# Kernel tuning notes

Hardware: AMD Instinct MI355X
Metric: run time of the kernel (lower is better)

## Reference

```python
import jax, jax.numpy as jnp
import numpy as np

PROCESSING_STEPS = 3


def setup_inputs() -> dict:
    key = jax.random.key(0)
    ks = jax.random.split(key, 8)
    B, N, d = 1024, 128, 128
    y = jax.random.normal(ks[0], (B, N, d), dtype=jnp.float32)
    lengths = jax.random.randint(ks[1], (B,), 1, N + 1, dtype=jnp.int32)
    s = 0.05
    W_ih = jax.random.normal(ks[2], (4 * d, 2 * d), dtype=jnp.float32) * s
    W_hh = jax.random.normal(ks[3], (4 * d, d), dtype=jnp.float32) * s
    b_ih = jax.random.normal(ks[4], (4 * d,), dtype=jnp.float32) * s
    b_hh = jax.random.normal(ks[5], (4 * d,), dtype=jnp.float32) * s
    W_m = jax.random.normal(ks[6], (1, 2 * d), dtype=jnp.float32) * s
    b_m = jax.random.normal(ks[7], (1,), dtype=jnp.float32) * s
    mean = jnp.zeros((1,), jnp.float32)
    stddev = jnp.ones((1,), jnp.float32)
    return {"y": y, "lengths": lengths, "W_ih": W_ih, "W_hh": W_hh,
            "b_ih": b_ih, "b_hh": b_hh, "W_m": W_m, "b_m": b_m,
            "mean": mean, "stddev": stddev}


def reference(y, lengths, W_ih, W_hh, b_ih, b_hh, W_m, b_m, mean, stddev):
    # y: [B, N, d] padded atomwise representation; lengths: valid atoms per molecule
    B, N, d = y.shape
    mask = jnp.arange(N)[None, :] < lengths[:, None]          # [B, N]
    maskf = mask.astype(y.dtype)[..., None]                    # [B, N, 1]
    neg_inf = jnp.finfo(y.dtype).min

    q_star = jnp.zeros((B, 2 * d), y.dtype)
    h = jnp.zeros((B, d), y.dtype)
    c = jnp.zeros((B, d), y.dtype)

    def step(carry, _):
        q_star, h, c = carry
        # single-layer LSTM cell (PyTorch gate order i, f, g, o)
        gates = q_star @ W_ih.T + b_ih + h @ W_hh.T + b_hh     # [B, 4d]
        i, f, g, o = jnp.split(gates, 4, axis=-1)
        c2 = jax.nn.sigmoid(f) * c + jax.nn.sigmoid(i) * jnp.tanh(g)
        h2 = jax.nn.sigmoid(o) * jnp.tanh(c2)
        q = h2                                                  # [B, d]
        # attention: gather q per atom, segment softmax, scatter_add
        e = jnp.einsum('bnd,bd->bn', y, q)                      # [B, N]
        e = jnp.where(mask, e, neg_inf)
        a = jax.nn.softmax(e, axis=-1)[..., None] * maskf       # [B, N, 1]
        r = jnp.sum(a * y, axis=1)                              # [B, d]
        return (jnp.concatenate([q, r], axis=-1), h2, c2), None

    (q_star, h, c), _ = jax.lax.scan(step, (q_star, h, c), None,
                                     length=PROCESSING_STEPS)
    out = q_star @ W_m.T + b_m                                  # [B, 1]
    return out * stddev + mean
```

## Files before the change

### kernel.cpp

```cpp
#include <hip/hip_runtime.h>
#include <math.h>

#define BB 1024
#define NN 128
#define DD 128

__device__ __forceinline__ float sigmoidf_(float x) { return 1.0f / (1.0f + expf(-x)); }

__global__ __launch_bounds__(256) void k_prep2(
    const float* __restrict__ W_ih, const float* __restrict__ W_hh,
    const float* __restrict__ b_ih, const float* __restrict__ b_hh,
    float* __restrict__ Wfull, float* __restrict__ gbase) {
  int b = blockIdx.x, t = threadIdx.x;
  if (b < 64) {
    int base = b * 2048;
    for (int i = t; i < 2048; i += 256) {
      int idx = base + i;
      int j = idx >> 8, d = idx & 255;
      float v = W_ih[(j << 8) + d];
      if (d < 128) v += W_hh[(j << 7) + d];
      Wfull[idx] = v;
    }
  } else {
    __shared__ float h1l[DD];
    if (t < DD) {
      float bi = b_ih[t] + b_hh[t];
      float bg = b_ih[256 + t] + b_hh[256 + t];
      float bo = b_ih[384 + t] + b_hh[384 + t];
      float cc = sigmoidf_(bi) * tanhf(bg);
      h1l[t] = sigmoidf_(bo) * tanhf(cc);
    }
    __syncthreads();
    int j0 = (b - 64) * 128;
    if (t < 128) {
      int j = j0 + t;
      float acc = b_ih[j] + b_hh[j];
      #pragma unroll 8
      for (int d = 0; d < DD; ++d)
        acc = fmaf(W_ih[(j << 8) + d] + W_hh[(j << 7) + d], h1l[d], acc);
      gbase[j] = acc;
    }
  }
}

struct SMX {
  float ql[2][DD];
  float c1l[DD];
  float rp[2][4][DD];
  float xcat[2][256];
  float g2[2][512];
  float c2l[2][DD];
  float redm[2][4], reds[2][4], redf[2][4];
};

__global__ __launch_bounds__(512, 4) void k_fused(
    const float* __restrict__ y, const int* __restrict__ lengths,
    const float* __restrict__ Wfull, const float* __restrict__ gbase,
    const float* __restrict__ b_ih, const float* __restrict__ b_hh,
    const float* __restrict__ Wm, const float* __restrict__ bm,
    const float* __restrict__ mn, const float* __restrict__ sd,
    float* __restrict__ out) {
  __shared__ SMX s;
  const int t = threadIdx.x;
  const int lane = t & 63;
  const int h = t >> 8;
  const int th = t & 255;
  const int w4 = (t >> 6) & 3;
  const int sub = lane & 15, g = lane >> 4;
  const int d0 = sub << 3;
  const int wbase = w4 << 2;
  const int m = h ? (1023 - (int)blockIdx.x) : (int)blockIdx.x;
  const int len = lengths[m];
  const float* yb = y + (size_t)m * (NN * DD);

  if (th < DD) {
    float bi = b_ih[th] + b_hh[th];
    float bg = b_ih[256 + th] + b_hh[256 + th];
    float bo = b_ih[384 + th] + b_hh[384 + th];
    float cc = sigmoidf_(bi) * tanhf(bg);
    s.ql[h][th] = sigmoidf_(bo) * tanhf(cc);
    if (h == 0) s.c1l[th] = cc;
  }

  float4 va[8], vb[8];
  #pragma unroll
  for (int it = 0; it < 8; ++it) {
    int n = (it << 4) + wbase + g;
    int nc = (n < len) ? n : (len - 1);
    const float4* yr = (const float4*)(yb + nc * DD + d0);
    va[it] = yr[0];
    vb[it] = yr[1];
  }
  __syncthreads();

  auto attn = [&](float* rdst, bool is_final) {
    float4 q0 = *(const float4*)&s.ql[h][d0];
    float4 q1 = *(const float4*)&s.ql[h][d0 + 4];
    float ee[8];
    #pragma unroll
    for (int it = 0; it < 8; ++it) {
      int nw = (it << 4) + wbase;
      if (nw < len) {
        int n = nw + g;
        float p = fmaf(va[it].x, q0.x, fmaf(va[it].y, q0.y,
                  fmaf(va[it].z, q0.z, fmaf(va[it].w, q0.w,
                  fmaf(vb[it].x, q1.x, fmaf(vb[it].y, q1.y,
                  fmaf(vb[it].z, q1.z, vb[it].w * q1.w)))))));
        #pragma unroll
        for (int sh = 1; sh < 16; sh <<= 1) p += __shfl_xor(p, sh, 64);
        ee[it] = (n < len) ? p : -3.0e38f;
      } else {
        ee[it] = -3.0e38f;
      }
    }
    float mloc = ee[0];
    #pragma unroll
    for (int it = 1; it < 8; ++it) mloc = fmaxf(mloc, ee[it]);
    #pragma unroll
    for (int sh = 1; sh < 64; sh <<= 1) mloc = fmaxf(mloc, __shfl_xor(mloc, sh, 64));
    float a[8], sl = 0.0f;
    #pragma unroll
    for (int it = 0; it < 8; ++it) { a[it] = expf(ee[it] - mloc); sl += a[it]; }
    #pragma unroll
    for (int sh = 1; sh < 64; sh <<= 1) sl += __shfl_xor(sl, sh, 64);
    if (lane == 0) { s.redm[h][w4] = mloc; s.reds[h][w4] = sl; }
    __syncthreads();
    float m0_ = s.redm[h][0], m1_ = s.redm[h][1], m2_ = s.redm[h][2], m3_ = s.redm[h][3];
    float mx = fmaxf(fmaxf(m0_, m1_), fmaxf(m2_, m3_));
    float Zraw = s.reds[h][0] * expf(m0_ - mx) + s.reds[h][1] * expf(m1_ - mx) +
                 s.reds[h][2] * expf(m2_ - mx) + s.reds[h][3] * expf(m3_ - mx);
    float wscale = expf(mloc - mx) * (16.0f / Zraw);

    float4 r0 = {0.f, 0.f, 0.f, 0.f}, r1 = {0.f, 0.f, 0.f, 0.f};
    #pragma unroll
    for (int it = 0; it < 8; ++it) {
      int nw = (it << 4) + wbase;
      if (nw < len) {
        float av = a[it];
        r0.x = fmaf(av, va[it].x, r0.x); r0.y = fmaf(av, va[it].y, r0.y);
        r0.z = fmaf(av, va[it].z, r0.z); r0.w = fmaf(av, va[it].w, r0.w);
        r1.x = fmaf(av, vb[it].x, r1.x); r1.y = fmaf(av, vb[it].y, r1.y);
        r1.z = fmaf(av, vb[it].z, r1.z); r1.w = fmaf(av, vb[it].w, r1.w);
      }
    }
    r0.x *= wscale; r0.y *= wscale; r0.z *= wscale; r0.w *= wscale;
    r1.x *= wscale; r1.y *= wscale; r1.z *= wscale; r1.w *= wscale;
    #pragma unroll
    for (int sh = 16; sh < 64; sh <<= 1) {
      r0.x += __shfl_xor(r0.x, sh, 64); r0.y += __shfl_xor(r0.y, sh, 64);
      r0.z += __shfl_xor(r0.z, sh, 64); r0.w += __shfl_xor(r0.w, sh, 64);
      r1.x += __shfl_xor(r1.x, sh, 64); r1.y += __shfl_xor(r1.y, sh, 64);
      r1.z += __shfl_xor(r1.z, sh, 64); r1.w += __shfl_xor(r1.w, sh, 64);
    }
    if (g == 0) {
      *(float4*)&s.rp[h][w4][d0] = r0;
      *(float4*)&s.rp[h][w4][d0 + 4] = r1;
    }
    __syncthreads();
    float r_ = 0.0f;
    if (th < DD) {
      r_ = s.rp[h][0][th] + s.rp[h][1][th] + s.rp[h][2][th] + s.rp[h][3][th];
      if (!is_final) rdst[th] = r_;
    }
    if (is_final) {
      float part = (th < DD) ? (Wm[th] * s.ql[h][th] + Wm[DD + th] * r_) : 0.0f;
      #pragma unroll
      for (int sh = 1; sh < 64; sh <<= 1) part += __shfl_xor(part, sh, 64);
      if (lane == 0) s.redf[h][w4] = part;
      __syncthreads();
      if (th == 0)
        out[m] = (s.redf[h][0] + s.redf[h][1] + s.redf[h][2] + s.redf[h][3] + bm[0])
                 * sd[0] + mn[0];
    } else {
      __syncthreads();
    }
  };

  attn(&s.xcat[h][128], false);

  {
    int j = t;
    float bA = gbase[j];
    float aA0 = bA, aA1 = 0.f, aB0 = bA, aB1 = 0.f;
    const float4* wr = (const float4*)(Wfull + (j << 8) + 128);
    const float4* xA = (const float4*)&s.xcat[0][128];
    const float4* xB = (const float4*)&s.xcat[1][128];
    #pragma unroll 2
    for (int k = 0; k < 32; k += 2) {
      float4 w0 = wr[k], w1 = wr[k + 1];
      float4 a0 = xA[k], a1 = xA[k + 1];
      float4 b0 = xB[k], b1 = xB[k + 1];
      aA0 = fmaf(w0.x, a0.x, fmaf(w0.y, a0.y, fmaf(w0.z, a0.z, fmaf(w0.w, a0.w, aA0))));
      aA1 = fmaf(w1.x, a1.x, fmaf(w1.y, a1.y, fmaf(w1.z, a1.z, fmaf(w1.w, a1.w, aA1))));
      aB0 = fmaf(w0.x, b0.x, fmaf(w0.y, b0.y, fmaf(w0.z, b0.z, fmaf(w0.w, b0.w, aB0))));
      aB1 = fmaf(w1.x, b1.x, fmaf(w1.y, b1.y, fmaf(w1.z, b1.z, fmaf(w1.w, b1.w, aB1))));
    }
    s.g2[0][j] = aA0 + aA1;
    s.g2[1][j] = aB0 + aB1;
  }
  __syncthreads();
  if (t < 256) {
    int mol = t >> 7, u = t & 127;
    float I = s.g2[mol][u], F = s.g2[mol][128 + u];
    float G = s.g2[mol][256 + u], O = s.g2[mol][384 + u];
    float cc = fmaf(sigmoidf_(F), s.c1l[u], sigmoidf_(I) * tanhf(G));
    float hh = sigmoidf_(O) * tanhf(cc);
    s.c2l[mol][u] = cc;
    s.xcat[mol][u] = hh;
    s.ql[mol][u] = hh;
  }
  __syncthreads();

  attn(&s.xcat[h][128], false);

  {
    int j = t;
    float bA = b_ih[j] + b_hh[j];
    float aA0 = bA, aA1 = 0.f, aB0 = bA, aB1 = 0.f;
    const float4* wr = (const float4*)(Wfull + (j << 8));
    const float4* xA = (const float4*)&s.xcat[0][0];
    const float4* xB = (const float4*)&s.xcat[1][0];
    #pragma unroll 2
    for (int k = 0; k < 64; k += 2) {
      float4 w0 = wr[k], w1 = wr[k + 1];
      float4 a0 = xA[k], a1 = xA[k + 1];
      float4 b0 = xB[k], b1 = xB[k + 1];
      aA0 = fmaf(w0.x, a0.x, fmaf(w0.y, a0.y, fmaf(w0.z, a0.z, fmaf(w0.w, a0.w, aA0))));
      aA1 = fmaf(w1.x, a1.x, fmaf(w1.y, a1.y, fmaf(w1.z, a1.z, fmaf(w1.w, a1.w, aA1))));
      aB0 = fmaf(w0.x, b0.x, fmaf(w0.y, b0.y, fmaf(w0.z, b0.z, fmaf(w0.w, b0.w, aB0))));
      aB1 = fmaf(w1.x, b1.x, fmaf(w1.y, b1.y, fmaf(w1.z, b1.z, fmaf(w1.w, b1.w, aB1))));
    }
    s.g2[0][j] = aA0 + aA1;
    s.g2[1][j] = aB0 + aB1;
  }
  __syncthreads();
  if (t < 256) {
    int mol = t >> 7, u = t & 127;
    float I = s.g2[mol][u], F = s.g2[mol][128 + u];
    float G = s.g2[mol][256 + u], O = s.g2[mol][384 + u];
    float cc = fmaf(sigmoidf_(F), s.c2l[mol][u], sigmoidf_(I) * tanhf(G));
    float hh = sigmoidf_(O) * tanhf(cc);
    s.ql[mol][u] = hh;
  }
  __syncthreads();

  attn(nullptr, true);
}

extern "C" void kernel_launch(void* const* d_in, const int* in_sizes, int n_in,
                              void* d_out, int out_size, void* d_ws, size_t ws_size,
                              hipStream_t stream) {
  const float* y    = (const float*)d_in[0];
  const int*   len  = (const int*)  d_in[1];
  const float* W_ih = (const float*)d_in[2];
  const float* W_hh = (const float*)d_in[3];
  const float* b_ih = (const float*)d_in[4];
  const float* b_hh = (const float*)d_in[5];
  const float* W_m  = (const float*)d_in[6];
  const float* b_m  = (const float*)d_in[7];
  const float* mean = (const float*)d_in[8];
  const float* sd   = (const float*)d_in[9];
  float* out = (float*)d_out;

  float* ws    = (float*)d_ws;
  float* Wfull = ws;
  float* gbase = ws + 131072;

  k_prep2<<<68, 256, 0, stream>>>(W_ih, W_hh, b_ih, b_hh, Wfull, gbase);
  k_fused<<<512, 512, 0, stream>>>(y, len, Wfull, gbase, b_ih, b_hh,
                                   W_m, b_m, mean, sd, out);
}
```

Before: 73.06 us.

## Use one molecule per block, drop softmax max pass, use fast exp/tanh

Splits the fused kernel from two molecules per 512-thread block into one molecule per 256-thread block, and rewrites the LSTM gate matvec as a cooperative warp-level dot product with shuffle reduction. Softmax no longer subtracts the running max, which removes a reduction and a barrier per attention step. This relies on logits staying small enough not to overflow exp. Sigmoid and tanh now use __expf-based fast approximations. The cost is doubling per-block weight traffic, since Wfull is no longer shared by two molecules, plus slight accuracy loss.

```diff
diff --git a/kernel.cpp b/kernel.cpp
--- a/kernel.cpp
+++ b/kernel.cpp
@@ -5,7 +5,8 @@
 #define NN 128
 #define DD 128
 
-__device__ __forceinline__ float sigmoidf_(float x) { return 1.0f / (1.0f + expf(-x)); }
+__device__ __forceinline__ float fsig_(float x)  { return 1.0f / (1.0f + __expf(-x)); }
+__device__ __forceinline__ float ftanh_(float x) { return 2.0f / (1.0f + __expf(-2.0f * x)) - 1.0f; }
 
 __global__ __launch_bounds__(256) void k_prep2(
     const float* __restrict__ W_ih, const float* __restrict__ W_hh,
@@ -27,8 +28,8 @@
       float bi = b_ih[t] + b_hh[t];
       float bg = b_ih[256 + t] + b_hh[256 + t];
       float bo = b_ih[384 + t] + b_hh[384 + t];
-      float cc = sigmoidf_(bi) * tanhf(bg);
-      h1l[t] = sigmoidf_(bo) * tanhf(cc);
+      float cc = fsig_(bi) * ftanh_(bg);
+      h1l[t] = fsig_(bo) * ftanh_(cc);
     }
     __syncthreads();
     int j0 = (b - 64) * 128;
@@ -44,16 +45,16 @@
 }
 
 struct SMX {
-  float ql[2][DD];
+  float ql[DD];
   float c1l[DD];
-  float rp[2][4][DD];
-  float xcat[2][256];
-  float g2[2][512];
-  float c2l[2][DD];
-  float redm[2][4], reds[2][4], redf[2][4];
+  float rp[4][DD];
+  float xcat[256];
+  float g2[512];
+  float c2l[DD];
+  float reds[4], redf[4];
 };
 
-__global__ __launch_bounds__(512, 4) void k_fused(
+__global__ __launch_bounds__(256, 4) void k_fused(
     const float* __restrict__ y, const int* __restrict__ lengths,
     const float* __restrict__ Wfull, const float* __restrict__ gbase,
     const float* __restrict__ b_ih, const float* __restrict__ b_hh,
@@ -62,24 +63,21 @@
     float* __restrict__ out) {
   __shared__ SMX s;
   const int t = threadIdx.x;
-  const int lane = t & 63;
-  const int h = t >> 8;
-  const int th = t & 255;
-  const int w4 = (t >> 6) & 3;
+  const int lane = t & 63, w = t >> 6;
   const int sub = lane & 15, g = lane >> 4;
   const int d0 = sub << 3;
-  const int wbase = w4 << 2;
-  const int m = h ? (1023 - (int)blockIdx.x) : (int)blockIdx.x;
+  const int wbase = w << 2;
+  const int m = blockIdx.x;
   const int len = lengths[m];
   const float* yb = y + (size_t)m * (NN * DD);
 
-  if (th < DD) {
-    float bi = b_ih[th] + b_hh[th];
-    float bg = b_ih[256 + th] + b_hh[256 + th];
-    float bo = b_ih[384 + th] + b_hh[384 + th];
-    float cc = sigmoidf_(bi) * tanhf(bg);
-    s.ql[h][th] = sigmoidf_(bo) * tanhf(cc);
-    if (h == 0) s.c1l[th] = cc;
+  if (t < DD) {
+    float bi = b_ih[t] + b_hh[t];
+    float bg = b_ih[256 + t] + b_hh[256 + t];
+    float bo = b_ih[384 + t] + b_hh[384 + t];
+    float cc = fsig_(bi) * ftanh_(bg);
+    s.c1l[t] = cc;
+    s.ql[t] = fsig_(bo) * ftanh_(cc);
   }
 
   float4 va[8], vb[8];
@@ -93,10 +91,10 @@
   }
   __syncthreads();
 
-  auto attn = [&](float* rdst, bool is_final) {
-    float4 q0 = *(const float4*)&s.ql[h][d0];
-    float4 q1 = *(const float4*)&s.ql[h][d0 + 4];
-    float ee[8];
+  auto attn = [&](bool is_final) {
+    float4 q0 = *(const float4*)&s.ql[d0];
+    float4 q1 = *(const float4*)&s.ql[d0 + 4];
+    float a[8], sl = 0.0f;
     #pragma unroll
     for (int it = 0; it < 8; ++it) {
       int nw = (it << 4) + wbase;
@@ -108,28 +106,17 @@
                   fmaf(vb[it].z, q1.z, vb[it].w * q1.w)))))));
         #pragma unroll
         for (int sh = 1; sh < 16; sh <<= 1) p += __shfl_xor(p, sh, 64);
-        ee[it] = (n < len) ? p : -3.0e38f;
+        a[it] = (n < len) ? __expf(p) : 0.0f;
       } else {
-        ee[it] = -3.0e38f;
-      }
-    }
-    float mloc = ee[0];
-    #pragma unroll
-    for (int it = 1; it < 8; ++it) mloc = fmaxf(mloc, ee[it]);
-    #pragma unroll
-    for (int sh = 1; sh < 64; sh <<= 1) mloc = fmaxf(mloc, __shfl_xor(mloc, sh, 64));
-    float a[8], sl = 0.0f;
-    #pragma unroll
-    for (int it = 0; it < 8; ++it) { a[it] = expf(ee[it] - mloc); sl += a[it]; }
+        a[it] = 0.0f;
+      }
+      sl += a[it];
+    }
     #pragma unroll
     for (int sh = 1; sh < 64; sh <<= 1) sl += __shfl_xor(sl, sh, 64);
-    if (lane == 0) { s.redm[h][w4] = mloc; s.reds[h][w4] = sl; }
-    __syncthreads();
-    float m0_ = s.redm[h][0], m1_ = s.redm[h][1], m2_ = s.redm[h][2], m3_ = s.redm[h][3];
-    float mx = fmaxf(fmaxf(m0_, m1_), fmaxf(m2_, m3_));
-    float Zraw = s.reds[h][0] * expf(m0_ - mx) + s.reds[h][1] * expf(m1_ - mx) +
-                 s.reds[h][2] * expf(m2_ - mx) + s.reds[h][3] * expf(m3_ - mx);
-    float wscale = expf(mloc - mx) * (16.0f / Zraw);
+    if (lane == 0) s.reds[w] = sl;
+    __syncthreads();
+    float wscale = 16.0f / (s.reds[0] + s.reds[1] + s.reds[2] + s.reds[3]);
 
     float4 r0 = {0.f, 0.f, 0.f, 0.f}, r1 = {0.f, 0.f, 0.f, 0.f};
     #pragma unroll
@@ -153,98 +140,71 @@
       r1.z += __shfl_xor(r1.z, sh, 64); r1.w += __shfl_xor(r1.w, sh, 64);
     }
     if (g == 0) {
-      *(float4*)&s.rp[h][w4][d0] = r0;
-      *(float4*)&s.rp[h][w4][d0 + 4] = r1;
-    }
-    __syncthreads();
-    float r_ = 0.0f;
-    if (th < DD) {
-      r_ = s.rp[h][0][th] + s.rp[h][1][th] + s.rp[h][2][th] + s.rp[h][3][th];
-      if (!is_final) rdst[th] = r_;
-    }
-    if (is_final) {
-      float part = (th < DD) ? (Wm[th] * s.ql[h][th] + Wm[DD + th] * r_) : 0.0f;
+      *(float4*)&s.rp[w][d0] = r0;
+      *(float4*)&s.rp[w][d0 + 4] = r1;
+    }
+    __syncthreads();
+    if (!is_final) {
+      if (t < DD) s.xcat[128 + t] = s.rp[0][t] + s.rp[1][t] + s.rp[2][t] + s.rp[3][t];
+      __syncthreads();
+    } else {
+      float part = 0.0f;
+      if (t < DD) {
+        float r_ = s.rp[0][t] + s.rp[1][t] + s.rp[2][t] + s.rp[3][t];
+        part = Wm[t] * s.ql[t] + Wm[DD + t] * r_;
+      }
       #pragma unroll
       for (int sh = 1; sh < 64; sh <<= 1) part += __shfl_xor(part, sh, 64);
-      if (lane == 0) s.redf[h][w4] = part;
+      if (lane == 0) s.redf[w] = part;
       __syncthreads();
-      if (th == 0)
-        out[m] = (s.redf[h][0] + s.redf[h][1] + s.redf[h][2] + s.redf[h][3] + bm[0])
-                 * sd[0] + mn[0];
-    } else {
-      __syncthreads();
+      if (t == 0)
+        out[m] = (s.redf[0] + s.redf[1] + s.redf[2] + s.redf[3] + bm[0]) * sd[0] + mn[0];
     }
   };
 
-  attn(&s.xcat[h][128], false);
-
-  {
-    int j = t;
-    float bA = gbase[j];
-    float aA0 = bA, aA1 = 0.f, aB0 = bA, aB1 = 0.f;
-    const float4* wr = (const float4*)(Wfull + (j << 8) + 128);
-    const float4* xA = (const float4*)&s.xcat[0][128];
-    const float4* xB = (const float4*)&s.xcat[1][128];
-    #pragma unroll 2
-    for (int k = 0; k < 32; k += 2) {
-      float4 w0 = wr[k], w1 = wr[k + 1];
-      float4 a0 = xA[k], a1 = xA[k + 1];
-      float4 b0 = xB[k], b1 = xB[k + 1];
-      aA0 = fmaf(w0.x, a0.x, fmaf(w0.y, a0.y, fmaf(w0.z, a0.z, fmaf(w0.w, a0.w, aA0))));
-      aA1 = fmaf(w1.x, a1.x, fmaf(w1.y, a1.y, fmaf(w1.z, a1.z, fmaf(w1.w, a1.w, aA1))));
-      aB0 = fmaf(w0.x, b0.x, fmaf(w0.y, b0.y, fmaf(w0.z, b0.z, fmaf(w0.w, b0.w, aB0))));
-      aB1 = fmaf(w1.x, b1.x, fmaf(w1.y, b1.y, fmaf(w1.z, b1.z, fmaf(w1.w, b1.w, aB1))));
-    }
-    s.g2[0][j] = aA0 + aA1;
-    s.g2[1][j] = aB0 + aB1;
-  }
+  auto matvec = [&](int qlo, const float* bias_g, bool use_gbase) {
+    #pragma unroll 4
+    for (int iter = 0; iter < 32; ++iter) {
+      int j = (iter << 4) + wbase + g;
+      const float4* wr = (const float4*)(Wfull + (j << 8));
+      float acc = 0.0f;
+      #pragma unroll
+      for (int q = 0; q < 4; ++q) {
+        if (q < qlo) continue;
+        int idx = (q << 4) + sub;
+        float4 wv = wr[idx];
+        float4 xa = *(const float4*)&s.xcat[idx << 2];
+        acc = fmaf(wv.x, xa.x, fmaf(wv.y, xa.y, fmaf(wv.z, xa.z, fmaf(wv.w, xa.w, acc))));
+      }
+      #pragma unroll
+      for (int sh = 1; sh < 16; sh <<= 1) acc += __shfl_xor(acc, sh, 64);
+      if (sub == 0)
+        s.g2[j] = acc + (use_gbase ? bias_g[j] : (b_ih[j] + b_hh[j]));
+    }
+  };
+
+  auto nonlin = [&](const float* cin_src, bool save_c) {
+    if (t < DD) {
+      float I = s.g2[t], F = s.g2[128 + t];
+      float G = s.g2[256 + t], O = s.g2[384 + t];
+      float cc = fmaf(fsig_(F), cin_src[t], fsig_(I) * ftanh_(G));
+      float hh = fsig_(O) * ftanh_(cc);
+      if (save_c) s.c2l[t] = cc;
+      s.xcat[t] = hh;
+      s.ql[t] = hh;
+    }
+    __syncthreads();
+  };
+
+  attn(false);
+  matvec(2, gbase, true);
   __syncthreads();
-  if (t < 256) {
-    int mol = t >> 7, u = t & 127;
-    float I = s.g2[mol][u], F = s.g2[mol][128 + u];
-    float G = s.g2[mol][256 + u], O = s.g2[mol][384 + u];
-    float cc = fmaf(sigmoidf_(F), s.c1l[u], sigmoidf_(I) * tanhf(G));
-    float hh = sigmoidf_(O) * tanhf(cc);
-    s.c2l[mol][u] = cc;
-    s.xcat[mol][u] = hh;
-    s.ql[mol][u] = hh;
-  }
+  nonlin(s.c1l, true);
+  attn(false);
+  matvec(0, nullptr, false);
   __syncthreads();
-
-  attn(&s.xcat[h][128], false);
-
-  {
-    int j = t;
-    float bA = b_ih[j] + b_hh[j];
-    float aA0 = bA, aA1 = 0.f, aB0 = bA, aB1 = 0.f;
-    const float4* wr = (const float4*)(Wfull + (j << 8));
-    const float4* xA = (const float4*)&s.xcat[0][0];
-    const float4* xB = (const float4*)&s.xcat[1][0];
-    #pragma unroll 2
-    for (int k = 0; k < 64; k += 2) {
-      float4 w0 = wr[k], w1 = wr[k + 1];
-      float4 a0 = xA[k], a1 = xA[k + 1];
-      float4 b0 = xB[k], b1 = xB[k + 1];
-      aA0 = fmaf(w0.x, a0.x, fmaf(w0.y, a0.y, fmaf(w0.z, a0.z, fmaf(w0.w, a0.w, aA0))));
-      aA1 = fmaf(w1.x, a1.x, fmaf(w1.y, a1.y, fmaf(w1.z, a1.z, fmaf(w1.w, a1.w, aA1))));
-      aB0 = fmaf(w0.x, b0.x, fmaf(w0.y, b0.y, fmaf(w0.z, b0.z, fmaf(w0.w, b0.w, aB0))));
-      aB1 = fmaf(w1.x, b1.x, fmaf(w1.y, b1.y, fmaf(w1.z, b1.z, fmaf(w1.w, b1.w, aB1))));
-    }
-    s.g2[0][j] = aA0 + aA1;
-    s.g2[1][j] = aB0 + aB1;
-  }
-  __syncthreads();
-  if (t < 256) {
-    int mol = t >> 7, u = t & 127;
-    float I = s.g2[mol][u], F = s.g2[mol][128 + u];
-    float G = s.g2[mol][256 + u], O = s.g2[mol][384 + u];
-    float cc = fmaf(sigmoidf_(F), s.c2l[mol][u], sigmoidf_(I) * tanhf(G));
-    float hh = sigmoidf_(O) * tanhf(cc);
-    s.ql[mol][u] = hh;
-  }
-  __syncthreads();
-
-  attn(nullptr, true);
+  nonlin(s.c2l, false);
+  attn(true);
 }
 
 extern "C" void kernel_launch(void* const* d_in, const int* in_sizes, int n_in,
@@ -267,6 +227,6 @@
   float* gbase = ws + 131072;
 
   k_prep2<<<68, 256, 0, stream>>>(W_ih, W_hh, b_ih, b_hh, Wfull, gbase);
-  k_fused<<<512, 512, 0, stream>>>(y, len, Wfull, gbase, b_ih, b_hh,
-                                   W_m, b_m, mean, sd, out);
+  k_fused<<<BB, 256, 0, stream>>>(y, len, Wfull, gbase, b_ih, b_hh,
+                                  W_m, b_m, mean, sd, out);
 }
```

After: 74.99 us. 1.03x slower.
